# Optimization experiments

Hardware: AMD Instinct MI355X
Metric: run time of the kernel (lower is better)

## Reference

```python
import jax, jax.numpy as jnp
import numpy as np

TEMPERATURE = 0.05
MIN_SCALE = 0.01
MAX_SCALE = 1.0 - 0.001
EPS = 1e-7

N_NODES = 200000
N_LEAVES = 100000
RANK = 128
N_PAIRS = 1000000


def setup_inputs() -> dict:
    key = jax.random.key(0)
    k1, k2, k3, k4, k5, k6 = jax.random.split(key, 6)
    # internal-node embedding table (dumpy_node init, tiny norms as in init_size)
    embeddings_weight = jax.random.normal(k1, (N_NODES, RANK), dtype=jnp.float32) * 0.001
    # leaf embeddings: points strictly inside the Poincare ball
    u = jax.random.normal(k2, (N_LEAVES, RANK), dtype=jnp.float32)
    radii = jax.random.uniform(k3, (N_LEAVES, 1), minval=0.1, maxval=0.9, dtype=jnp.float32)
    leaves_embeddings = u / (jnp.linalg.norm(u, axis=1, keepdims=True) + 1e-6) * radii
    lca = jax.random.randint(k4, (1,), 0, N_NODES)
    l_idx = jax.random.randint(k5, (N_PAIRS,), 0, N_LEAVES)
    r_idx = jax.random.randint(k6, (N_PAIRS,), 0, N_LEAVES)
    sims = jax.random.uniform(jax.random.fold_in(key, 7), (N_PAIRS,), dtype=jnp.float32)
    scale = jnp.array([0.5], dtype=jnp.float32)
    return {"lca": lca, "l_idx": l_idx, "r_idx": r_idx, "sims": sims,
            "embeddings_weight": embeddings_weight,
            "leaves_embeddings": leaves_embeddings, "scale": scale}


def _hyp_dist(x, y):
    # Poincare-ball distance. x: [1, r], y: [P, r] -> [P]
    sq = jnp.sum((x - y) ** 2, axis=-1)
    nx = jnp.sum(x * x, axis=-1)
    ny = jnp.sum(y * y, axis=-1)
    arg = 1.0 + 2.0 * sq / ((1.0 - nx) * (1.0 - ny))
    return jnp.arccosh(jnp.clip(arg, 1.0 + EPS))


def reference(lca, l_idx, r_idx, sims, embeddings_weight, leaves_embeddings, scale):
    # embedding gather + L2-normalize * clamped scale
    e1 = embeddings_weight[lca]                             # [1, r]
    s = jnp.clip(scale, MIN_SCALE, MAX_SCALE)
    e1 = e1 / jnp.maximum(jnp.linalg.norm(e1, axis=1, keepdims=True), 1e-12) * s
    # vectorized hyperbolic pair distances (the original's Python loop)
    d = _hyp_dist(e1, leaves_embeddings[l_idx]) + _hyp_dist(e1, leaves_embeddings[r_idx])  # [P]
    weights = jax.nn.softmax(d / TEMPERATURE, axis=-1)
    w_ord = jnp.sum(sims * weights, axis=-1, keepdims=True)
    total = jnp.sum(sims, axis=-1, keepdims=True) - w_ord
    return jnp.mean(total)
```

## Files before the change

kernel.cpp:

```cpp
#include <hip/hip_runtime.h>
#include <math.h>

#define RANK 128
#define INV_T 20.0f
#define EPS_ARG 1e-7f
#define NBLK_PAIR 512
#define NTHR 256

__device__ inline void comb(float& m, float& z, float& w, float& s,
                            float m2, float z2, float w2, float s2) {
    float mn = fmaxf(m, m2);
    float a = (m  == mn) ? 1.0f : __expf(m  - mn);
    float b = (m2 == mn) ? 1.0f : __expf(m2 - mn);
    z = z * a + z2 * b;
    w = w * a + w2 * b;
    m = mn;
    s += s2;
}

__global__ void k_leaf(const float* __restrict__ emb, const int* __restrict__ lca,
                       const float* __restrict__ scale,
                       const float4* __restrict__ leaves,
                       float* __restrict__ D, int nLeaves) {
    __shared__ float4 se1[RANK / 4];
    __shared__ float  snx[2];
    int t = threadIdx.x;

    if (t < 32) {
        float4 v = ((const float4*)(emb + (size_t)lca[0] * RANK))[t];
        float sq = v.x * v.x + v.y * v.y + v.z * v.z + v.w * v.w;
#pragma unroll
        for (int o = 16; o; o >>= 1) sq += __shfl_down(sq, o, 32);
        sq = __shfl(sq, 0, 32);
        float bn = sqrtf(sq);
        float s = fminf(fmaxf(scale[0], 0.01f), 1.0f - 0.001f);
        float k = s / fmaxf(bn, 1e-12f);
        float4 e; e.x = v.x * k; e.y = v.y * k; e.z = v.z * k; e.w = v.w * k;
        se1[t] = e;
        float sq2 = e.x * e.x + e.y * e.y + e.z * e.z + e.w * e.w;
#pragma unroll
        for (int o = 16; o; o >>= 1) sq2 += __shfl_down(sq2, o, 32);
        if (t == 0) {
            snx[0] = sq2;
            snx[1] = 1.0f / (1.0f - sq2);
        }
    }
    __syncthreads();

    int lane = t & 63, wid = t >> 6;
    int l31 = lane & 31, half = lane >> 5;
    int wavesPerBlock = NTHR >> 6;
    int gw = blockIdx.x * wavesPerBlock + wid;
    int nw = gridDim.x * wavesPerBlock;
    float nx = snx[0], invdx = snx[1];
    float4 e = se1[l31];
    for (int jj = gw; 2 * jj < nLeaves; jj += nw) {
        int j = 2 * jj + half;
        float dot = 0.0f, ny = 0.0f;
        if (j < nLeaves) {
            float4 y = leaves[(size_t)j * (RANK / 4) + l31];
            dot = y.x * e.x + y.y * e.y + y.z * e.z + y.w * e.w;
            ny  = y.x * y.x + y.y * y.y + y.z * y.z + y.w * y.w;
        }
#pragma unroll
        for (int o = 16; o; o >>= 1) {
            dot += __shfl_down(dot, o, 32);
            ny  += __shfl_down(ny, o, 32);
        }
        if (l31 == 0 && j < nLeaves) {
            float sq  = nx + ny - 2.0f * dot;
            float arg = 1.0f + 2.0f * sq * invdx / (1.0f - ny);
            arg = fmaxf(arg, 1.0f + EPS_ARG);
            D[j] = acoshf(arg);
        }
    }
}

__global__ void k_pair(const int* __restrict__ li, const int* __restrict__ ri,
                       const float* __restrict__ sims, const float* __restrict__ D,
                       float4* __restrict__ partials, int P) {
    float m = -INFINITY, z = 0.0f, w = 0.0f, s = 0.0f;
    int tid = blockIdx.x * NTHR + threadIdx.x;
    int nthreads = gridDim.x * NTHR;
    int P4 = P >> 2;
    const int4*   li4 = (const int4*)li;
    const int4*   ri4 = (const int4*)ri;
    const float4* s4p = (const float4*)sims;
    for (int i = tid; i < P4; i += nthreads) {
        int4 l = li4[i], r = ri4[i];
        float4 sv = s4p[i];
        float a0 = D[l.x], b0 = D[r.x];
        float a1 = D[l.y], b1 = D[r.y];
        float a2 = D[l.z], b2 = D[r.z];
        float a3 = D[l.w], b3 = D[r.w];
        float t0 = (a0 + b0) * INV_T, t1 = (a1 + b1) * INV_T;
        float t2 = (a2 + b2) * INV_T, t3 = (a3 + b3) * INV_T;
#define STEP(tp, svv)                                                  \
        if (tp <= m) { float e = __expf(tp - m); z += e; w = fmaf(svv, e, w); } \
        else { float rr = __expf(m - tp); z = fmaf(z, rr, 1.0f); w = fmaf(w, rr, svv); m = tp; } \
        s += svv;
        STEP(t0, sv.x) STEP(t1, sv.y) STEP(t2, sv.z) STEP(t3, sv.w)
    }
    int tail0 = P4 << 2;
    for (int p = tail0 + tid; p < P; p += nthreads) {
        float tp = (D[li[p]] + D[ri[p]]) * INV_T;
        float svv = sims[p];
        STEP(tp, svv)
    }
#undef STEP
#pragma unroll
    for (int o = 32; o; o >>= 1) {
        float m2 = __shfl_xor(m, o), z2 = __shfl_xor(z, o);
        float w2 = __shfl_xor(w, o), s2 = __shfl_xor(s, o);
        comb(m, z, w, s, m2, z2, w2, s2);
    }
    __shared__ float4 sp[NTHR / 64];
    int lane = threadIdx.x & 63, wid = threadIdx.x >> 6;
    if (lane == 0) sp[wid] = make_float4(m, z, w, s);
    __syncthreads();
    if (threadIdx.x == 0) {
        for (int i = 1; i < (NTHR >> 6); i++) {
            float4 q = sp[i];
            comb(m, z, w, s, q.x, q.y, q.z, q.w);
        }
        partials[blockIdx.x] = make_float4(m, z, w, s);
    }
}

__global__ void k_fin(const float4* __restrict__ partials, float* __restrict__ out, int nb) {
    int t = threadIdx.x;
    float m = -INFINITY, z = 0.0f, w = 0.0f, s = 0.0f;
    for (int i = t; i < nb; i += blockDim.x) {
        float4 q = partials[i];
        comb(m, z, w, s, q.x, q.y, q.z, q.w);
    }
#pragma unroll
    for (int o = 32; o; o >>= 1) {
        float m2 = __shfl_xor(m, o), z2 = __shfl_xor(z, o);
        float w2 = __shfl_xor(w, o), s2 = __shfl_xor(s, o);
        comb(m, z, w, s, m2, z2, w2, s2);
    }
    __shared__ float4 sp[4];
    int lane = t & 63, wid = t >> 6;
    if (lane == 0) sp[wid] = make_float4(m, z, w, s);
    __syncthreads();
    if (t == 0) {
        for (int i = 1; i < (int)(blockDim.x >> 6); i++) {
            float4 q = sp[i];
            comb(m, z, w, s, q.x, q.y, q.z, q.w);
        }
        out[0] = s - w / z;
    }
}

extern "C" void kernel_launch(void* const* d_in, const int* in_sizes, int n_in,
                              void* d_out, int out_size, void* d_ws, size_t ws_size,
                              hipStream_t stream) {
    const int*   lca    = (const int*)d_in[0];
    const int*   li     = (const int*)d_in[1];
    const int*   ri     = (const int*)d_in[2];
    const float* sims   = (const float*)d_in[3];
    const float* emb    = (const float*)d_in[4];
    const float* leaves = (const float*)d_in[5];
    const float* scale  = (const float*)d_in[6];
    float* out = (float*)d_out;

    int P       = in_sizes[1];
    int nLeaves = in_sizes[5] / RANK;

    char* ws = (char*)d_ws;
    float*  D        = (float*)ws;
    size_t  poff     = (((size_t)nLeaves * sizeof(float) + 1023) / 1024) * 1024;
    float4* partials = (float4*)(ws + poff);

    k_leaf<<<2048, NTHR, 0, stream>>>(emb, lca, scale, (const float4*)leaves, D, nLeaves);
    k_pair<<<NBLK_PAIR, NTHR, 0, stream>>>(li, ri, sims, D, partials, P);
    k_fin <<<1, NTHR, 0, stream>>>(partials, out, NBLK_PAIR);
}
```

Before: 195.7 us.

## Fuse leaf, pair and final reduction into one cooperative kernel with grid syncs

Merges the three kernels into one cooperative launch of 1024 blocks that uses grid.sync between the leaf-distance phase, the pair softmax-reduction phase and the final combine. The leaf loop now handles two leaves per half-wave per iteration to raise memory-level parallelism. The aim is to remove two kernel launch gaps and tail effects. In exchange it adds grid-wide barrier cost, needs all 1024 blocks co-resident, and leaves most blocks idle during the final combine.

```diff
diff --git a/kernel.cpp b/kernel.cpp
--- a/kernel.cpp
+++ b/kernel.cpp
@@ -1,10 +1,13 @@
 #include <hip/hip_runtime.h>
+#include <hip/hip_cooperative_groups.h>
 #include <math.h>
+
+namespace cg = cooperative_groups;
 
 #define RANK 128
 #define INV_T 20.0f
 #define EPS_ARG 1e-7f
-#define NBLK_PAIR 512
+#define NBLK 1024
 #define NTHR 256
 
 __device__ inline void comb(float& m, float& z, float& w, float& s,
@@ -18,12 +21,18 @@
     s += s2;
 }
 
-__global__ void k_leaf(const float* __restrict__ emb, const int* __restrict__ lca,
-                       const float* __restrict__ scale,
-                       const float4* __restrict__ leaves,
-                       float* __restrict__ D, int nLeaves) {
+__global__ __launch_bounds__(NTHR, 4)
+void fused(const float* __restrict__ emb, const int* __restrict__ lca,
+           const float* __restrict__ scale, const float4* __restrict__ leaves,
+           float* __restrict__ D, int nLeaves,
+           const int* __restrict__ li, const int* __restrict__ ri,
+           const float* __restrict__ sims, float4* __restrict__ partials,
+           int P, float* __restrict__ out)
+{
+    cg::grid_group grid = cg::this_grid();
     __shared__ float4 se1[RANK / 4];
     __shared__ float  snx[2];
+    __shared__ float4 sp[NTHR / 64];
     int t = threadIdx.x;
 
     if (t < 32) {
@@ -47,122 +56,137 @@
     }
     __syncthreads();
 
-    int lane = t & 63, wid = t >> 6;
-    int l31 = lane & 31, half = lane >> 5;
-    int wavesPerBlock = NTHR >> 6;
-    int gw = blockIdx.x * wavesPerBlock + wid;
-    int nw = gridDim.x * wavesPerBlock;
-    float nx = snx[0], invdx = snx[1];
-    float4 e = se1[l31];
-    for (int jj = gw; 2 * jj < nLeaves; jj += nw) {
-        int j = 2 * jj + half;
-        float dot = 0.0f, ny = 0.0f;
-        if (j < nLeaves) {
-            float4 y = leaves[(size_t)j * (RANK / 4) + l31];
-            dot = y.x * e.x + y.y * e.y + y.z * e.z + y.w * e.w;
-            ny  = y.x * y.x + y.y * y.y + y.z * y.z + y.w * y.w;
-        }
-#pragma unroll
-        for (int o = 16; o; o >>= 1) {
-            dot += __shfl_down(dot, o, 32);
-            ny  += __shfl_down(ny, o, 32);
-        }
-        if (l31 == 0 && j < nLeaves) {
-            float sq  = nx + ny - 2.0f * dot;
-            float arg = 1.0f + 2.0f * sq * invdx / (1.0f - ny);
-            arg = fmaxf(arg, 1.0f + EPS_ARG);
-            D[j] = acoshf(arg);
-        }
-    }
-}
-
-__global__ void k_pair(const int* __restrict__ li, const int* __restrict__ ri,
-                       const float* __restrict__ sims, const float* __restrict__ D,
-                       float4* __restrict__ partials, int P) {
+    {
+        int lane = t & 63, wid = t >> 6;
+        int l31 = lane & 31, half = lane >> 5;
+        int gw = blockIdx.x * (NTHR >> 6) + wid;
+        int nw = NBLK * (NTHR >> 6);
+        float nx = snx[0], invdx = snx[1];
+        float4 e = se1[l31];
+        for (int jj = gw; 4 * jj < nLeaves; jj += nw) {
+            int j0 = 4 * jj + half;
+            int j1 = j0 + 2;
+            bool v0 = j0 < nLeaves, v1 = j1 < nLeaves;
+            float4 y0 = make_float4(0.f, 0.f, 0.f, 0.f);
+            float4 y1 = make_float4(0.f, 0.f, 0.f, 0.f);
+            if (v0) y0 = leaves[(size_t)j0 * (RANK / 4) + l31];
+            if (v1) y1 = leaves[(size_t)j1 * (RANK / 4) + l31];
+            float dot0 = y0.x * e.x + y0.y * e.y + y0.z * e.z + y0.w * e.w;
+            float ny0  = y0.x * y0.x + y0.y * y0.y + y0.z * y0.z + y0.w * y0.w;
+            float dot1 = y1.x * e.x + y1.y * e.y + y1.z * e.z + y1.w * e.w;
+            float ny1  = y1.x * y1.x + y1.y * y1.y + y1.z * y1.z + y1.w * y1.w;
+#pragma unroll
+            for (int o = 16; o; o >>= 1) {
+                dot0 += __shfl_down(dot0, o, 32);
+                ny0  += __shfl_down(ny0, o, 32);
+                dot1 += __shfl_down(dot1, o, 32);
+                ny1  += __shfl_down(ny1, o, 32);
+            }
+            if (l31 == 0) {
+                if (v0) {
+                    float sq  = nx + ny0 - 2.0f * dot0;
+                    float arg = 1.0f + 2.0f * sq * invdx / (1.0f - ny0);
+                    D[j0] = acoshf(fmaxf(arg, 1.0f + EPS_ARG));
+                }
+                if (v1) {
+                    float sq  = nx + ny1 - 2.0f * dot1;
+                    float arg = 1.0f + 2.0f * sq * invdx / (1.0f - ny1);
+                    D[j1] = acoshf(fmaxf(arg, 1.0f + EPS_ARG));
+                }
+            }
+        }
+    }
+    __threadfence();
+    grid.sync();
+
     float m = -INFINITY, z = 0.0f, w = 0.0f, s = 0.0f;
-    int tid = blockIdx.x * NTHR + threadIdx.x;
-    int nthreads = gridDim.x * NTHR;
-    int P4 = P >> 2;
-    const int4*   li4 = (const int4*)li;
-    const int4*   ri4 = (const int4*)ri;
-    const float4* s4p = (const float4*)sims;
-    for (int i = tid; i < P4; i += nthreads) {
-        int4 l = li4[i], r = ri4[i];
-        float4 sv = s4p[i];
-        float a0 = D[l.x], b0 = D[r.x];
-        float a1 = D[l.y], b1 = D[r.y];
-        float a2 = D[l.z], b2 = D[r.z];
-        float a3 = D[l.w], b3 = D[r.w];
-        float t0 = (a0 + b0) * INV_T, t1 = (a1 + b1) * INV_T;
-        float t2 = (a2 + b2) * INV_T, t3 = (a3 + b3) * INV_T;
+    {
+        int tid = blockIdx.x * NTHR + t;
+        const int nthreads = NBLK * NTHR;
+        int P4 = P >> 2;
+        const int4*   li4 = (const int4*)li;
+        const int4*   ri4 = (const int4*)ri;
+        const float4* s4p = (const float4*)sims;
+        for (int i = tid; i < P4; i += nthreads) {
+            int4 l = li4[i], r = ri4[i];
+            float4 sv = s4p[i];
+            float a0 = D[l.x], b0 = D[r.x];
+            float a1 = D[l.y], b1 = D[r.y];
+            float a2 = D[l.z], b2 = D[r.z];
+            float a3 = D[l.w], b3 = D[r.w];
+            float t0 = (a0 + b0) * INV_T, t1 = (a1 + b1) * INV_T;
+            float t2 = (a2 + b2) * INV_T, t3 = (a3 + b3) * INV_T;
 #define STEP(tp, svv)                                                  \
-        if (tp <= m) { float e = __expf(tp - m); z += e; w = fmaf(svv, e, w); } \
-        else { float rr = __expf(m - tp); z = fmaf(z, rr, 1.0f); w = fmaf(w, rr, svv); m = tp; } \
-        s += svv;
-        STEP(t0, sv.x) STEP(t1, sv.y) STEP(t2, sv.z) STEP(t3, sv.w)
-    }
-    int tail0 = P4 << 2;
-    for (int p = tail0 + tid; p < P; p += nthreads) {
-        float tp = (D[li[p]] + D[ri[p]]) * INV_T;
-        float svv = sims[p];
-        STEP(tp, svv)
-    }
+            if (tp <= m) { float e = __expf(tp - m); z += e; w = fmaf(svv, e, w); } \
+            else { float rr = __expf(m - tp); z = fmaf(z, rr, 1.0f); w = fmaf(w, rr, svv); m = tp; } \
+            s += svv;
+            STEP(t0, sv.x) STEP(t1, sv.y) STEP(t2, sv.z) STEP(t3, sv.w)
+        }
+        int tail0 = P4 << 2;
+        for (int p = tail0 + tid; p < P; p += nthreads) {
+            float tp = (D[li[p]] + D[ri[p]]) * INV_T;
+            float svv = sims[p];
+            STEP(tp, svv)
+        }
 #undef STEP
+    }
 #pragma unroll
     for (int o = 32; o; o >>= 1) {
         float m2 = __shfl_xor(m, o), z2 = __shfl_xor(z, o);
         float w2 = __shfl_xor(w, o), s2 = __shfl_xor(s, o);
         comb(m, z, w, s, m2, z2, w2, s2);
     }
-    __shared__ float4 sp[NTHR / 64];
-    int lane = threadIdx.x & 63, wid = threadIdx.x >> 6;
-    if (lane == 0) sp[wid] = make_float4(m, z, w, s);
-    __syncthreads();
-    if (threadIdx.x == 0) {
-        for (int i = 1; i < (NTHR >> 6); i++) {
-            float4 q = sp[i];
-            comb(m, z, w, s, q.x, q.y, q.z, q.w);
-        }
-        partials[blockIdx.x] = make_float4(m, z, w, s);
-    }
-}
-
-__global__ void k_fin(const float4* __restrict__ partials, float* __restrict__ out, int nb) {
-    int t = threadIdx.x;
-    float m = -INFINITY, z = 0.0f, w = 0.0f, s = 0.0f;
-    for (int i = t; i < nb; i += blockDim.x) {
-        float4 q = partials[i];
-        comb(m, z, w, s, q.x, q.y, q.z, q.w);
-    }
-#pragma unroll
-    for (int o = 32; o; o >>= 1) {
-        float m2 = __shfl_xor(m, o), z2 = __shfl_xor(z, o);
-        float w2 = __shfl_xor(w, o), s2 = __shfl_xor(s, o);
-        comb(m, z, w, s, m2, z2, w2, s2);
-    }
-    __shared__ float4 sp[4];
-    int lane = t & 63, wid = t >> 6;
-    if (lane == 0) sp[wid] = make_float4(m, z, w, s);
-    __syncthreads();
-    if (t == 0) {
-        for (int i = 1; i < (int)(blockDim.x >> 6); i++) {
-            float4 q = sp[i];
-            comb(m, z, w, s, q.x, q.y, q.z, q.w);
-        }
-        out[0] = s - w / z;
+    {
+        int lane = t & 63, wid = t >> 6;
+        if (lane == 0) sp[wid] = make_float4(m, z, w, s);
+        __syncthreads();
+        if (t == 0) {
+            for (int i = 1; i < (NTHR >> 6); i++) {
+                float4 q = sp[i];
+                comb(m, z, w, s, q.x, q.y, q.z, q.w);
+            }
+            partials[blockIdx.x] = make_float4(m, z, w, s);
+        }
+    }
+    __threadfence();
+    grid.sync();
+
+    if (blockIdx.x == 0) {
+        float fm = -INFINITY, fz = 0.0f, fw = 0.0f, fs = 0.0f;
+        for (int i = t; i < NBLK; i += NTHR) {
+            float4 q = partials[i];
+            comb(fm, fz, fw, fs, q.x, q.y, q.z, q.w);
+        }
+#pragma unroll
+        for (int o = 32; o; o >>= 1) {
+            float m2 = __shfl_xor(fm, o), z2 = __shfl_xor(fz, o);
+            float w2 = __shfl_xor(fw, o), s2 = __shfl_xor(fs, o);
+            comb(fm, fz, fw, fs, m2, z2, w2, s2);
+        }
+        int lane = t & 63, wid = t >> 6;
+        __syncthreads();
+        if (lane == 0) sp[wid] = make_float4(fm, fz, fw, fs);
+        __syncthreads();
+        if (t == 0) {
+            for (int i = 1; i < (NTHR >> 6); i++) {
+                float4 q = sp[i];
+                comb(fm, fz, fw, fs, q.x, q.y, q.z, q.w);
+            }
+            out[0] = fs - fw / fz;
+        }
     }
 }
 
 extern "C" void kernel_launch(void* const* d_in, const int* in_sizes, int n_in,
                               void* d_out, int out_size, void* d_ws, size_t ws_size,
                               hipStream_t stream) {
+    const float* emb    = (const float*)d_in[4];
     const int*   lca    = (const int*)d_in[0];
+    const float* scale  = (const float*)d_in[6];
+    const float4* leaves = (const float4*)d_in[5];
     const int*   li     = (const int*)d_in[1];
     const int*   ri     = (const int*)d_in[2];
     const float* sims   = (const float*)d_in[3];
-    const float* emb    = (const float*)d_in[4];
-    const float* leaves = (const float*)d_in[5];
-    const float* scale  = (const float*)d_in[6];
     float* out = (float*)d_out;
 
     int P       = in_sizes[1];
@@ -173,7 +197,9 @@
     size_t  poff     = (((size_t)nLeaves * sizeof(float) + 1023) / 1024) * 1024;
     float4* partials = (float4*)(ws + poff);
 
-    k_leaf<<<2048, NTHR, 0, stream>>>(emb, lca, scale, (const float4*)leaves, D, nLeaves);
-    k_pair<<<NBLK_PAIR, NTHR, 0, stream>>>(li, ri, sims, D, partials, P);
-    k_fin <<<1, NTHR, 0, stream>>>(partials, out, NBLK_PAIR);
+    void* args[] = { (void*)&emb, (void*)&lca, (void*)&scale, (void*)&leaves,
+                     (void*)&D, (void*)&nLeaves, (void*)&li, (void*)&ri,
+                     (void*)&sims, (void*)&partials, (void*)&P, (void*)&out };
+    hipLaunchCooperativeKernel((const void*)fused, dim3(NBLK), dim3(NTHR),
+                               args, 0, stream);
 }
```

After: 610.8 us. 212% more time.
